# Kernel optimization log

Hardware: AMD Instinct MI355X
Metric: run time of the kernel (lower is better)

Reference implementation:

```python
import jax, jax.numpy as jnp
import numpy as np

N, H, E = 40000, 128, 640000
BN_EPS = 1e-5


def setup_inputs() -> dict:
    key = jax.random.key(0)
    ks = jax.random.split(key, 5)
    x = jax.random.normal(ks[0], (N, H), dtype=jnp.float32)
    edge_index = jax.random.randint(ks[1], (2, E), 0, N, dtype=jnp.int64)
    eps = jnp.zeros((1,), dtype=jnp.float32)
    s = 1.0 / np.sqrt(H)  # torch Linear init scale
    W1 = jax.random.uniform(ks[2], (H, H), jnp.float32, -s, s)
    b1 = jnp.zeros((H,), dtype=jnp.float32)
    W2 = jax.random.uniform(ks[3], (H, H), jnp.float32, -s, s)
    b2 = jnp.zeros((H,), dtype=jnp.float32)
    gamma = jnp.ones((H,), dtype=jnp.float32)
    beta = jnp.zeros((H,), dtype=jnp.float32)
    return {"x": x, "edge_index": edge_index, "eps": eps,
            "W1": W1, "b1": b1, "W2": W2, "b2": b2,
            "gamma": gamma, "beta": beta}


def reference(x, edge_index, eps, W1, b1, W2, b2, gamma, beta):
    src = edge_index[0]
    tgt = edge_index[1]
    # gather source features, scatter-add into target rows: [N, H]
    agg = jax.ops.segment_sum(x[src], tgt, num_segments=x.shape[0])
    out = agg + (1.0 + eps) * x
    # MLP: Linear -> ReLU -> Linear -> BatchNorm1d (train mode) -> ReLU
    h = jax.nn.relu(out @ W1.T + b1)
    h = h @ W2.T + b2
    mean = jnp.mean(h, axis=0)
    var = jnp.mean((h - mean) ** 2, axis=0)  # biased var, as BN uses
    h = (h - mean) * jax.lax.rsqrt(var + BN_EPS) * gamma + beta
    return jax.nn.relu(h)
```

## Files before the change

kernel.cpp:

```cpp
#include <hip/hip_runtime.h>

#define HDIM 128
#define BN_EPS 1e-5f
#define SCAN_BINS 1024
#define NPART 8
#define LSTR 136

typedef short short8 __attribute__((ext_vector_type(8)));
typedef float floatx4 __attribute__((ext_vector_type(4)));

__device__ __forceinline__ unsigned short f2b(float f) {
    union { float f; unsigned u; } v; v.f = f;
    unsigned r = v.u + 0x7FFFu + ((v.u >> 16) & 1u);
    return (unsigned short)(r >> 16);
}

__device__ __forceinline__ float b2f(unsigned short b) {
    union { unsigned u; float f; } v; v.u = (unsigned)b << 16;
    return v.f;
}

__global__ __launch_bounds__(256) void prep_kernel(
    const float* __restrict__ x, unsigned short* __restrict__ xB, long n4,
    const float* __restrict__ W1, const float* __restrict__ W2,
    unsigned short* __restrict__ W1B, unsigned short* __restrict__ W2B,
    const int* __restrict__ eidx, int* __restrict__ hist,
    int* __restrict__ rank, int E)
{
    int tid = blockIdx.x * 256 + threadIdx.x;
    int stride = gridDim.x * 256;
    for (long i = tid; i < n4; i += stride) {
        float4 v = ((const float4*)x)[i];
        ushort4 o;
        o.x = f2b(v.x); o.y = f2b(v.y); o.z = f2b(v.z); o.w = f2b(v.w);
        ((ushort4*)xB)[i] = o;
    }
    for (int i = tid; i < HDIM * HDIM; i += stride) {
        W1B[i] = f2b(W1[i]);
        W2B[i] = f2b(W2[i]);
    }
    for (int e = tid; e < E; e += stride) {
        rank[e] = atomicAdd(&hist[eidx[E + e]], 1);
    }
}

__global__ __launch_bounds__(256) void block_scan_kernel(
    const int* __restrict__ hist, int* __restrict__ offsets,
    int* __restrict__ blockSums, float* __restrict__ statSum, int N)
{
    __shared__ int ts[256];
    int b = blockIdx.x, t = threadIdx.x;
    if (b == 0 && t < 2 * HDIM) statSum[t] = 0.f;
    int base = b * SCAN_BINS + t * 4;
    int4 h = make_int4(0, 0, 0, 0);
    if (base + 3 < N) {
        h = *(const int4*)(hist + base);
    } else {
        if (base + 0 < N) h.x = hist[base + 0];
        if (base + 1 < N) h.y = hist[base + 1];
        if (base + 2 < N) h.z = hist[base + 2];
    }
    int s = h.x + h.y + h.z + h.w;
    ts[t] = s;
    __syncthreads();
    for (int off = 1; off < 256; off <<= 1) {
        int v = ts[t];
        int add = (t >= off) ? ts[t - off] : 0;
        __syncthreads();
        ts[t] = v + add;
        __syncthreads();
    }
    int excl = ts[t] - s;
    int4 o;
    o.x = excl;
    o.y = o.x + h.x;
    o.z = o.y + h.y;
    o.w = o.z + h.z;
    if (base + 3 < N) {
        *(int4*)(offsets + base) = o;
    } else {
        if (base + 0 < N) offsets[base + 0] = o.x;
        if (base + 1 < N) offsets[base + 1] = o.y;
        if (base + 2 < N) offsets[base + 2] = o.z;
    }
    if (t == 255) blockSums[b] = ts[255];
}

__global__ __launch_bounds__(256) void scan_finalize_kernel(
    const int* __restrict__ blockSums, int* __restrict__ offsets, int N, int NB)
{
    __shared__ int ts[256];
    int b = blockIdx.x, t = threadIdx.x;
    ts[t] = (t < NB) ? blockSums[t] : 0;
    __syncthreads();
    for (int off = 1; off < 256; off <<= 1) {
        int v = ts[t];
        int add = (t >= off) ? ts[t - off] : 0;
        __syncthreads();
        ts[t] = v + add;
        __syncthreads();
    }
    int prefix = (b == 0) ? 0 : ts[b - 1];
    if (b == 0 && t == 0) offsets[N] = ts[NB - 1];
    int base = b * SCAN_BINS + t * 4;
    if (base + 3 < N) {
        int4 o = *(int4*)(offsets + base);
        o.x += prefix; o.y += prefix; o.z += prefix; o.w += prefix;
        *(int4*)(offsets + base) = o;
    } else {
        for (int j = 0; j < 4; j++) {
            int i = base + j;
            if (i < N) offsets[i] += prefix;
        }
    }
}

__global__ __launch_bounds__(256) void reorder_kernel(
    const int* __restrict__ eidx, const int* __restrict__ offsets,
    const int* __restrict__ rank, int* __restrict__ srcSorted,
    int E, int partSize)
{
    int part = blockIdx.x & (NPART - 1);
    int bi = blockIdx.x >> 3;
    int nb = gridDim.x >> 3;
    int lo = part * partSize;
    int hi = lo + partSize;
    int stride = nb * 256;
    for (int e = bi * 256 + threadIdx.x; e < E; e += stride) {
        int t = eidx[E + e];
        if (t >= lo && t < hi) {
            srcSorted[offsets[t] + rank[e]] = eidx[e];
        }
    }
}

__global__ __launch_bounds__(256, 4) void mega_kernel(
    const float* __restrict__ x, const unsigned short* __restrict__ xB,
    const int* __restrict__ offsets, const int* __restrict__ srcSorted,
    const float* __restrict__ eps,
    const unsigned short* __restrict__ W1B, const float* __restrict__ b1,
    const unsigned short* __restrict__ W2B, const float* __restrict__ b2,
    float* __restrict__ out, float* __restrict__ statSum,
    float* __restrict__ statSqs, int N)
{
    __shared__ unsigned short sT[64 * LSTR];
    __shared__ float sSum[HDIM];
    __shared__ float sSqs[HDIM];

    int tid = threadIdx.x;
    int rb = blockIdx.x * 64;
    if (tid < HDIM) { sSum[tid] = 0.f; sSqs[tid] = 0.f; }

    float coef = 1.0f + eps[0];
    int tx = tid & 15, ty = tid >> 4;
    int col = tx * 8;
    for (int g = 0; g < 4; g++) {
        int r = g * 16 + ty;
        int row = rb + r;
        float acc[8] = {0.f, 0.f, 0.f, 0.f, 0.f, 0.f, 0.f, 0.f};
        if (row < N) {
            float4 xv0 = *(const float4*)(x + (size_t)row * HDIM + col);
            float4 xv1 = *(const float4*)(x + (size_t)row * HDIM + col + 4);
            acc[0] = coef * xv0.x; acc[1] = coef * xv0.y;
            acc[2] = coef * xv0.z; acc[3] = coef * xv0.w;
            acc[4] = coef * xv1.x; acc[5] = coef * xv1.y;
            acc[6] = coef * xv1.z; acc[7] = coef * xv1.w;
            int beg = offsets[row], end = offsets[row + 1];
            int e = beg;
            for (; e + 7 < end; e += 8) {
                short8 u[8];
                #pragma unroll
                for (int q = 0; q < 8; q++) {
                    int s = srcSorted[e + q];
                    u[q] = *(const short8*)(xB + (size_t)s * HDIM + col);
                }
                #pragma unroll
                for (int q = 0; q < 8; q++)
                    #pragma unroll
                    for (int j = 0; j < 8; j++)
                        acc[j] += b2f((unsigned short)u[q][j]);
            }
            for (; e < end; e++) {
                int s = srcSorted[e];
                short8 u = *(const short8*)(xB + (size_t)s * HDIM + col);
                #pragma unroll
                for (int j = 0; j < 8; j++)
                    acc[j] += b2f((unsigned short)u[j]);
            }
        }
        short8 o;
        #pragma unroll
        for (int j = 0; j < 8; j++) o[j] = (short)f2b(acc[j]);
        *(short8*)(sT + r * LSTR + col) = o;
    }
    __syncthreads();

    int w = tid >> 6;
    int l = tid & 63;
    int m = l & 15, quad = l >> 4;
    unsigned short* myT = sT + w * 16 * LSTR;

    floatx4 acc1[8];
    #pragma unroll
    for (int t = 0; t < 8; t++) acc1[t] = (floatx4){0.f, 0.f, 0.f, 0.f};
    #pragma unroll
    for (int kk = 0; kk < 4; kk++) {
        int k0 = kk * 32 + quad * 8;
        short8 a = *(const short8*)(myT + m * LSTR + k0);
        #pragma unroll
        for (int t = 0; t < 8; t++) {
            short8 bfr = *(const short8*)(W1B + (size_t)(t * 16 + m) * HDIM + k0);
            acc1[t] = __builtin_amdgcn_mfma_f32_16x16x32_bf16(a, bfr, acc1[t], 0, 0, 0);
        }
    }
    #pragma unroll
    for (int t = 0; t < 8; t++) {
        int colc = t * 16 + m;
        float bs = b1[colc];
        #pragma unroll
        for (int r = 0; r < 4; r++) {
            float v = fmaxf(acc1[t][r] + bs, 0.f);
            myT[(quad * 4 + r) * LSTR + colc] = f2b(v);
        }
    }

    floatx4 acc2[8];
    #pragma unroll
    for (int t = 0; t < 8; t++) acc2[t] = (floatx4){0.f, 0.f, 0.f, 0.f};
    #pragma unroll
    for (int kk = 0; kk < 4; kk++) {
        int k0 = kk * 32 + quad * 8;
        short8 a = *(const short8*)(myT + m * LSTR + k0);
        #pragma unroll
        for (int t = 0; t < 8; t++) {
            short8 bfr = *(const short8*)(W2B + (size_t)(t * 16 + m) * HDIM + k0);
            acc2[t] = __builtin_amdgcn_mfma_f32_16x16x32_bf16(a, bfr, acc2[t], 0, 0, 0);
        }
    }
    int row0 = rb + w * 16 + quad * 4;
    #pragma unroll
    for (int t = 0; t < 8; t++) {
        int colc = t * 16 + m;
        float bs = b2[colc];
        float cs = 0.f, cq = 0.f;
        #pragma unroll
        for (int r = 0; r < 4; r++) {
            int row = row0 + r;
            if (row < N) {
                float v = acc2[t][r] + bs;
                out[(size_t)row * HDIM + colc] = v;
                cs += v; cq += v * v;
            }
        }
        cs += __shfl_xor(cs, 16, 64);
        cs += __shfl_xor(cs, 32, 64);
        cq += __shfl_xor(cq, 16, 64);
        cq += __shfl_xor(cq, 32, 64);
        if (quad == 0) {
            atomicAdd(&sSum[colc], cs);
            atomicAdd(&sSqs[colc], cq);
        }
    }
    __syncthreads();
    if (tid < HDIM) {
        atomicAdd(&statSum[tid], sSum[tid]);
        atomicAdd(&statSqs[tid], sSqs[tid]);
    }
}

__global__ __launch_bounds__(256) void bn_apply_kernel(
    float* __restrict__ out, const float* __restrict__ statSum,
    const float* __restrict__ statSqs, const float* __restrict__ gamma,
    const float* __restrict__ beta, int N, long n4)
{
    __shared__ float sSc[HDIM];
    __shared__ float sSh[HDIM];
    int t = threadIdx.x;
    if (t < HDIM) {
        float invN = 1.0f / (float)N;
        float mean = statSum[t] * invN;
        float var = statSqs[t] * invN - mean * mean;
        float sc = gamma[t] * rsqrtf(var + BN_EPS);
        sSc[t] = sc;
        sSh[t] = beta[t] - mean * sc;
    }
    __syncthreads();
    long stride = (long)gridDim.x * 256;
    for (long i = (long)blockIdx.x * 256 + t; i < n4; i += stride) {
        int cg = (int)(i & 31) * 4;
        float4 v = ((float4*)out)[i];
        v.x = fmaxf(v.x * sSc[cg + 0] + sSh[cg + 0], 0.f);
        v.y = fmaxf(v.y * sSc[cg + 1] + sSh[cg + 1], 0.f);
        v.z = fmaxf(v.z * sSc[cg + 2] + sSh[cg + 2], 0.f);
        v.w = fmaxf(v.w * sSc[cg + 3] + sSh[cg + 3], 0.f);
        ((float4*)out)[i] = v;
    }
}

extern "C" void kernel_launch(void* const* d_in, const int* in_sizes, int n_in,
                              void* d_out, int out_size, void* d_ws, size_t ws_size,
                              hipStream_t stream) {
    const float* x     = (const float*)d_in[0];
    const int*   eidx  = (const int*)d_in[1];
    const float* eps   = (const float*)d_in[2];
    const float* W1    = (const float*)d_in[3];
    const float* b1    = (const float*)d_in[4];
    const float* W2    = (const float*)d_in[5];
    const float* b2    = (const float*)d_in[6];
    const float* gamma = (const float*)d_in[7];
    const float* beta  = (const float*)d_in[8];
    float* out = (float*)d_out;

    int N = in_sizes[0] / HDIM;
    int E = in_sizes[1] / 2;
    size_t NH = (size_t)N * HDIM;
    int NB = (N + SCAN_BINS - 1) / SCAN_BINS;
    int NpadOff = (N + 1 + 3) & ~3;
    int partSize = (N + NPART - 1) / NPART;
    long n4 = (long)NH / 4;

    unsigned short* xB   = (unsigned short*)d_ws;
    unsigned short* W1B  = xB + NH;
    unsigned short* W2B  = W1B + HDIM * HDIM;
    float* statSum = (float*)(W2B + HDIM * HDIM);
    float* statSqs = statSum + HDIM;
    int*   hist    = (int*)(statSqs + HDIM);
    int*   offsets = hist + N;
    int*   rank    = offsets + NpadOff;
    int*   srcSorted = rank + E;
    int*   blockSums = srcSorted + E;

    hipMemsetAsync(hist, 0, (size_t)N * sizeof(int), stream);
    prep_kernel<<<1280, 256, 0, stream>>>(x, xB, n4, W1, W2, W1B, W2B, eidx, hist, rank, E);
    block_scan_kernel<<<NB, 256, 0, stream>>>(hist, offsets, blockSums, statSum, N);
    scan_finalize_kernel<<<NB, 256, 0, stream>>>(blockSums, offsets, N, NB);
    reorder_kernel<<<2048, 256, 0, stream>>>(eidx, offsets, rank, srcSorted, E, partSize);
    int gblocks = (N + 63) / 64;
    mega_kernel<<<gblocks, 256, 0, stream>>>(
        x, xB, offsets, srcSorted, eps, W1B, b1, W2B, b2,
        out, statSum, statSqs, N);
    bn_apply_kernel<<<2048, 256, 0, stream>>>(
        out, statSum, statSqs, gamma, beta, N, n4);
}
```

Baseline: 201.4 us.

## Slab-partition bf16 features for gather locality and merge scan kernels

Stores the bf16 copy of x as four 32-column slabs ([slab][node][32]). The aggregation kernel now gives each row to 4 lanes that walk all edges once per slab, so each slab pass touches a smaller working set that can stay in cache. The self term now reads the bf16 slab instead of fp32 x, which adds rounding on that term. The two-pass scan becomes a single kernel where each block recomputes its prefix by summing the earlier histogram entries, dropping a launch at the cost of redundant reads.

```diff
diff --git a/kernel.cpp b/kernel.cpp
--- a/kernel.cpp
+++ b/kernel.cpp
@@ -4,6 +4,7 @@
 #define BN_EPS 1e-5f
 #define SCAN_BINS 1024
 #define NPART 8
+#define NSLAB 4
 #define LSTR 136
 
 typedef short short8 __attribute__((ext_vector_type(8)));
@@ -21,7 +22,7 @@
 }
 
 __global__ __launch_bounds__(256) void prep_kernel(
-    const float* __restrict__ x, unsigned short* __restrict__ xB, long n4,
+    const float* __restrict__ x, unsigned short* __restrict__ xS, int N,
     const float* __restrict__ W1, const float* __restrict__ W2,
     unsigned short* __restrict__ W1B, unsigned short* __restrict__ W2B,
     const int* __restrict__ eidx, int* __restrict__ hist,
@@ -29,11 +30,22 @@
 {
     int tid = blockIdx.x * 256 + threadIdx.x;
     int stride = gridDim.x * 256;
-    for (long i = tid; i < n4; i += stride) {
-        float4 v = ((const float4*)x)[i];
-        ushort4 o;
-        o.x = f2b(v.x); o.y = f2b(v.y); o.z = f2b(v.z); o.w = f2b(v.w);
-        ((ushort4*)xB)[i] = o;
+    long n8 = (long)N * (HDIM / 8);
+    for (long i = tid; i < n8; i += stride) {
+        int n = (int)(i >> 4);
+        int u = (int)(i & 15);
+        int c = u * 8;
+        int s = c >> 5;
+        int off = c & 31;
+        const float* src = x + (size_t)n * HDIM + c;
+        float4 v0 = *(const float4*)(src);
+        float4 v1 = *(const float4*)(src + 4);
+        short8 o;
+        o[0] = (short)f2b(v0.x); o[1] = (short)f2b(v0.y);
+        o[2] = (short)f2b(v0.z); o[3] = (short)f2b(v0.w);
+        o[4] = (short)f2b(v1.x); o[5] = (short)f2b(v1.y);
+        o[6] = (short)f2b(v1.z); o[7] = (short)f2b(v1.w);
+        *(short8*)(xS + ((size_t)s * N + n) * 32 + off) = o;
     }
     for (int i = tid; i < HDIM * HDIM; i += stride) {
         W1B[i] = f2b(W1[i]);
@@ -44,13 +56,26 @@
     }
 }
 
-__global__ __launch_bounds__(256) void block_scan_kernel(
+__global__ __launch_bounds__(256) void scan_kernel(
     const int* __restrict__ hist, int* __restrict__ offsets,
-    int* __restrict__ blockSums, float* __restrict__ statSum, int N)
+    float* __restrict__ statSum, int N, int NB)
 {
     __shared__ int ts[256];
     int b = blockIdx.x, t = threadIdx.x;
     if (b == 0 && t < 2 * HDIM) statSum[t] = 0.f;
+
+    int lim = b * SCAN_BINS;
+    int pre = 0;
+    for (int i = t; i < lim; i += 256) pre += hist[i];
+    ts[t] = pre;
+    __syncthreads();
+    for (int off = 128; off > 0; off >>= 1) {
+        if (t < off) ts[t] += ts[t + off];
+        __syncthreads();
+    }
+    int blockPrefix = ts[0];
+    __syncthreads();
+
     int base = b * SCAN_BINS + t * 4;
     int4 h = make_int4(0, 0, 0, 0);
     if (base + 3 < N) {
@@ -70,7 +95,7 @@
         ts[t] = v + add;
         __syncthreads();
     }
-    int excl = ts[t] - s;
+    int excl = blockPrefix + ts[t] - s;
     int4 o;
     o.x = excl;
     o.y = o.x + h.x;
@@ -83,36 +108,7 @@
         if (base + 1 < N) offsets[base + 1] = o.y;
         if (base + 2 < N) offsets[base + 2] = o.z;
     }
-    if (t == 255) blockSums[b] = ts[255];
-}
-
-__global__ __launch_bounds__(256) void scan_finalize_kernel(
-    const int* __restrict__ blockSums, int* __restrict__ offsets, int N, int NB)
-{
-    __shared__ int ts[256];
-    int b = blockIdx.x, t = threadIdx.x;
-    ts[t] = (t < NB) ? blockSums[t] : 0;
-    __syncthreads();
-    for (int off = 1; off < 256; off <<= 1) {
-        int v = ts[t];
-        int add = (t >= off) ? ts[t - off] : 0;
-        __syncthreads();
-        ts[t] = v + add;
-        __syncthreads();
-    }
-    int prefix = (b == 0) ? 0 : ts[b - 1];
-    if (b == 0 && t == 0) offsets[N] = ts[NB - 1];
-    int base = b * SCAN_BINS + t * 4;
-    if (base + 3 < N) {
-        int4 o = *(int4*)(offsets + base);
-        o.x += prefix; o.y += prefix; o.z += prefix; o.w += prefix;
-        *(int4*)(offsets + base) = o;
-    } else {
-        for (int j = 0; j < 4; j++) {
-            int i = base + j;
-            if (i < N) offsets[i] += prefix;
-        }
-    }
+    if (b == NB - 1 && t == 255) offsets[N] = blockPrefix + ts[255];
 }
 
 __global__ __launch_bounds__(256) void reorder_kernel(
@@ -135,7 +131,7 @@
 }
 
 __global__ __launch_bounds__(256, 4) void mega_kernel(
-    const float* __restrict__ x, const unsigned short* __restrict__ xB,
+    const unsigned short* __restrict__ xS,
     const int* __restrict__ offsets, const int* __restrict__ srcSorted,
     const float* __restrict__ eps,
     const unsigned short* __restrict__ W1B, const float* __restrict__ b1,
@@ -152,46 +148,49 @@
     if (tid < HDIM) { sSum[tid] = 0.f; sSqs[tid] = 0.f; }
 
     float coef = 1.0f + eps[0];
-    int tx = tid & 15, ty = tid >> 4;
-    int col = tx * 8;
-    for (int g = 0; g < 4; g++) {
-        int r = g * 16 + ty;
-        int row = rb + r;
+    int rloc = tid >> 2;
+    int lane4 = tid & 3;
+    int cis = lane4 * 8;
+    int row = rb + rloc;
+    int beg = 0, end = 0;
+    if (row < N) { beg = offsets[row]; end = offsets[row + 1]; }
+
+    #pragma unroll
+    for (int s = 0; s < NSLAB; s++) {
+        const unsigned short* slab = xS + (size_t)s * N * 32;
         float acc[8] = {0.f, 0.f, 0.f, 0.f, 0.f, 0.f, 0.f, 0.f};
+        int e = beg;
+        for (; e + 3 < end; e += 4) {
+            int i0 = srcSorted[e];
+            int i1 = srcSorted[e + 1];
+            int i2 = srcSorted[e + 2];
+            int i3 = srcSorted[e + 3];
+            short8 u0 = *(const short8*)(slab + (size_t)i0 * 32 + cis);
+            short8 u1 = *(const short8*)(slab + (size_t)i1 * 32 + cis);
+            short8 u2 = *(const short8*)(slab + (size_t)i2 * 32 + cis);
+            short8 u3 = *(const short8*)(slab + (size_t)i3 * 32 + cis);
+            #pragma unroll
+            for (int j = 0; j < 8; j++)
+                acc[j] += (b2f((unsigned short)u0[j]) + b2f((unsigned short)u1[j]))
+                        + (b2f((unsigned short)u2[j]) + b2f((unsigned short)u3[j]));
+        }
+        for (; e < end; e++) {
+            int si = srcSorted[e];
+            short8 u = *(const short8*)(slab + (size_t)si * 32 + cis);
+            #pragma unroll
+            for (int j = 0; j < 8; j++)
+                acc[j] += b2f((unsigned short)u[j]);
+        }
         if (row < N) {
-            float4 xv0 = *(const float4*)(x + (size_t)row * HDIM + col);
-            float4 xv1 = *(const float4*)(x + (size_t)row * HDIM + col + 4);
-            acc[0] = coef * xv0.x; acc[1] = coef * xv0.y;
-            acc[2] = coef * xv0.z; acc[3] = coef * xv0.w;
-            acc[4] = coef * xv1.x; acc[5] = coef * xv1.y;
-            acc[6] = coef * xv1.z; acc[7] = coef * xv1.w;
-            int beg = offsets[row], end = offsets[row + 1];
-            int e = beg;
-            for (; e + 7 < end; e += 8) {
-                short8 u[8];
-                #pragma unroll
-                for (int q = 0; q < 8; q++) {
-                    int s = srcSorted[e + q];
-                    u[q] = *(const short8*)(xB + (size_t)s * HDIM + col);
-                }
-                #pragma unroll
-                for (int q = 0; q < 8; q++)
-                    #pragma unroll
-                    for (int j = 0; j < 8; j++)
-                        acc[j] += b2f((unsigned short)u[q][j]);
-            }
-            for (; e < end; e++) {
-                int s = srcSorted[e];
-                short8 u = *(const short8*)(xB + (size_t)s * HDIM + col);
-                #pragma unroll
-                for (int j = 0; j < 8; j++)
-                    acc[j] += b2f((unsigned short)u[j]);
-            }
+            short8 us = *(const short8*)(slab + (size_t)row * 32 + cis);
+            #pragma unroll
+            for (int j = 0; j < 8; j++)
+                acc[j] += coef * b2f((unsigned short)us[j]);
         }
         short8 o;
         #pragma unroll
         for (int j = 0; j < 8; j++) o[j] = (short)f2b(acc[j]);
-        *(short8*)(sT + r * LSTR + col) = o;
+        *(short8*)(sT + rloc * LSTR + s * 32 + cis) = o;
     }
     __syncthreads();
 
@@ -245,10 +244,10 @@
         float cs = 0.f, cq = 0.f;
         #pragma unroll
         for (int r = 0; r < 4; r++) {
-            int row = row0 + r;
-            if (row < N) {
+            int rw = row0 + r;
+            if (rw < N) {
                 float v = acc2[t][r] + bs;
-                out[(size_t)row * HDIM + colc] = v;
+                out[(size_t)rw * HDIM + colc] = v;
                 cs += v; cq += v * v;
             }
         }
@@ -319,8 +318,8 @@
     int partSize = (N + NPART - 1) / NPART;
     long n4 = (long)NH / 4;
 
-    unsigned short* xB   = (unsigned short*)d_ws;
-    unsigned short* W1B  = xB + NH;
+    unsigned short* xS   = (unsigned short*)d_ws;
+    unsigned short* W1B  = xS + NH;
     unsigned short* W2B  = W1B + HDIM * HDIM;
     float* statSum = (float*)(W2B + HDIM * HDIM);
     float* statSqs = statSum + HDIM;
@@ -328,16 +327,14 @@
     int*   offsets = hist + N;
     int*   rank    = offsets + NpadOff;
     int*   srcSorted = rank + E;
-    int*   blockSums = srcSorted + E;
 
     hipMemsetAsync(hist, 0, (size_t)N * sizeof(int), stream);
-    prep_kernel<<<1280, 256, 0, stream>>>(x, xB, n4, W1, W2, W1B, W2B, eidx, hist, rank, E);
-    block_scan_kernel<<<NB, 256, 0, stream>>>(hist, offsets, blockSums, statSum, N);
-    scan_finalize_kernel<<<NB, 256, 0, stream>>>(blockSums, offsets, N, NB);
+    prep_kernel<<<1280, 256, 0, stream>>>(x, xS, N, W1, W2, W1B, W2B, eidx, hist, rank, E);
+    scan_kernel<<<NB, 256, 0, stream>>>(hist, offsets, statSum, N, NB);
     reorder_kernel<<<2048, 256, 0, stream>>>(eidx, offsets, rank, srcSorted, E, partSize);
     int gblocks = (N + 63) / 64;
     mega_kernel<<<gblocks, 256, 0, stream>>>(
-        x, xB, offsets, srcSorted, eps, W1B, b1, W2B, b2,
+        xS, offsets, srcSorted, eps, W1B, b1, W2B, b2,
         out, statSum, statSqs, N);
     bn_apply_kernel<<<2048, 256, 0, stream>>>(
         out, statSum, statSqs, gamma, beta, N, n4);
```

Result: slower. 219.3 us (+8.9%).

## Fuse CSR prefix scan into reorder kernel and read bf16 self features

Applied to the files above, without the earlier changes.

The two-pass block scan and finalize kernels plus the separate reorder kernel are replaced, when a partition fits in shared memory, by one kernel in which each block recomputes its partition's prefix and offsets in LDS and then scatters source indices using those LDS offsets. This removes two launches and the global offsets round trip during reorder, at the cost of redundant histogram reads across blocks. The mega kernel now takes the self term from the bf16 copy of x instead of fp32 x, which halves that read but reduces precision of the (1+eps)*x term. Zeroing of the BN stats moves into prep_kernel.

```diff
diff --git a/kernel.cpp b/kernel.cpp
--- a/kernel.cpp
+++ b/kernel.cpp
@@ -4,6 +4,7 @@
 #define BN_EPS 1e-5f
 #define SCAN_BINS 1024
 #define NPART 8
+#define MAXPART 5120
 #define LSTR 136
 
 typedef short short8 __attribute__((ext_vector_type(8)));
@@ -25,10 +26,11 @@
     const float* __restrict__ W1, const float* __restrict__ W2,
     unsigned short* __restrict__ W1B, unsigned short* __restrict__ W2B,
     const int* __restrict__ eidx, int* __restrict__ hist,
-    int* __restrict__ rank, int E)
+    int* __restrict__ rank, float* __restrict__ statSum, int E)
 {
     int tid = blockIdx.x * 256 + threadIdx.x;
     int stride = gridDim.x * 256;
+    if (tid < 2 * HDIM) statSum[tid] = 0.f;
     for (long i = tid; i < n4; i += stride) {
         float4 v = ((const float4*)x)[i];
         ushort4 o;
@@ -44,13 +46,85 @@
     }
 }
 
-__global__ __launch_bounds__(256) void block_scan_kernel(
-    const int* __restrict__ hist, int* __restrict__ offsets,
-    int* __restrict__ blockSums, float* __restrict__ statSum, int N)
-{
+__global__ __launch_bounds__(256) void scan_reorder_kernel(
+    const int* __restrict__ hist, const int* __restrict__ eidx,
+    const int* __restrict__ rank, int* __restrict__ offsets,
+    int* __restrict__ srcSorted, int N, int E, int partSize)
+{
+    __shared__ int sOff[MAXPART];
     __shared__ int ts[256];
     int b = blockIdx.x, t = threadIdx.x;
-    if (b == 0 && t < 2 * HDIM) statSum[t] = 0.f;
+    int part = b & (NPART - 1);
+    int bi = b >> 3;
+    int nb = gridDim.x >> 3;
+    int lo = part * partSize;
+    int hi = lo + partSize; if (hi > N) hi = N;
+    int len = hi - lo;
+
+    int pre = 0;
+    for (int i = t; i < lo; i += 256) pre += hist[i];
+    ts[t] = pre;
+    __syncthreads();
+    for (int off = 128; off > 0; off >>= 1) {
+        if (t < off) ts[t] += ts[t + off];
+        __syncthreads();
+    }
+    int prefix = ts[0];
+    __syncthreads();
+
+    for (int i = t; i < len; i += 256) sOff[i] = hist[lo + i];
+    __syncthreads();
+
+    int chunk = (len + 255) / 256;
+    int clo = t * chunk;
+    int chi = clo + chunk; if (chi > len) chi = len;
+    int s = 0;
+    for (int i = clo; i < chi; i++) s += sOff[i];
+    ts[t] = s;
+    __syncthreads();
+    for (int off = 1; off < 256; off <<= 1) {
+        int v = ts[t];
+        int add = (t >= off) ? ts[t - off] : 0;
+        __syncthreads();
+        ts[t] = v + add;
+        __syncthreads();
+    }
+    int excl = prefix + ts[t] - s;
+    for (int i = clo; i < chi; i++) {
+        int v = sOff[i];
+        sOff[i] = excl;
+        if (bi == 0) offsets[lo + i] = excl;
+        excl += v;
+    }
+    if (bi == 0 && part == NPART - 1 && t == 0) offsets[N] = E;
+    __syncthreads();
+
+    int stride = nb * 256;
+    for (int e = bi * 256 + t; e < E; e += stride) {
+        int tg = eidx[E + e];
+        if (tg >= lo && tg < hi) {
+            srcSorted[sOff[tg - lo] + rank[e]] = eidx[e];
+        }
+    }
+}
+
+__global__ __launch_bounds__(256) void scan_kernel(
+    const int* __restrict__ hist, int* __restrict__ offsets,
+    int N, int NB)
+{
+    __shared__ int ts[256];
+    int b = blockIdx.x, t = threadIdx.x;
+    int lim = b * SCAN_BINS;
+    int pre = 0;
+    for (int i = t; i < lim; i += 256) pre += hist[i];
+    ts[t] = pre;
+    __syncthreads();
+    for (int off = 128; off > 0; off >>= 1) {
+        if (t < off) ts[t] += ts[t + off];
+        __syncthreads();
+    }
+    int blockPrefix = ts[0];
+    __syncthreads();
     int base = b * SCAN_BINS + t * 4;
     int4 h = make_int4(0, 0, 0, 0);
     if (base + 3 < N) {
@@ -70,7 +144,7 @@
         ts[t] = v + add;
         __syncthreads();
     }
-    int excl = ts[t] - s;
+    int excl = blockPrefix + ts[t] - s;
     int4 o;
     o.x = excl;
     o.y = o.x + h.x;
@@ -83,36 +157,7 @@
         if (base + 1 < N) offsets[base + 1] = o.y;
         if (base + 2 < N) offsets[base + 2] = o.z;
     }
-    if (t == 255) blockSums[b] = ts[255];
-}
-
-__global__ __launch_bounds__(256) void scan_finalize_kernel(
-    const int* __restrict__ blockSums, int* __restrict__ offsets, int N, int NB)
-{
-    __shared__ int ts[256];
-    int b = blockIdx.x, t = threadIdx.x;
-    ts[t] = (t < NB) ? blockSums[t] : 0;
-    __syncthreads();
-    for (int off = 1; off < 256; off <<= 1) {
-        int v = ts[t];
-        int add = (t >= off) ? ts[t - off] : 0;
-        __syncthreads();
-        ts[t] = v + add;
-        __syncthreads();
-    }
-    int prefix = (b == 0) ? 0 : ts[b - 1];
-    if (b == 0 && t == 0) offsets[N] = ts[NB - 1];
-    int base = b * SCAN_BINS + t * 4;
-    if (base + 3 < N) {
-        int4 o = *(int4*)(offsets + base);
-        o.x += prefix; o.y += prefix; o.z += prefix; o.w += prefix;
-        *(int4*)(offsets + base) = o;
-    } else {
-        for (int j = 0; j < 4; j++) {
-            int i = base + j;
-            if (i < N) offsets[i] += prefix;
-        }
-    }
+    if (b == NB - 1 && t == 255) offsets[N] = blockPrefix + ts[255];
 }
 
 __global__ __launch_bounds__(256) void reorder_kernel(
@@ -135,7 +180,7 @@
 }
 
 __global__ __launch_bounds__(256, 4) void mega_kernel(
-    const float* __restrict__ x, const unsigned short* __restrict__ xB,
+    const unsigned short* __restrict__ xB,
     const int* __restrict__ offsets, const int* __restrict__ srcSorted,
     const float* __restrict__ eps,
     const unsigned short* __restrict__ W1B, const float* __restrict__ b1,
@@ -159,12 +204,9 @@
         int row = rb + r;
         float acc[8] = {0.f, 0.f, 0.f, 0.f, 0.f, 0.f, 0.f, 0.f};
         if (row < N) {
-            float4 xv0 = *(const float4*)(x + (size_t)row * HDIM + col);
-            float4 xv1 = *(const float4*)(x + (size_t)row * HDIM + col + 4);
-            acc[0] = coef * xv0.x; acc[1] = coef * xv0.y;
-            acc[2] = coef * xv0.z; acc[3] = coef * xv0.w;
-            acc[4] = coef * xv1.x; acc[5] = coef * xv1.y;
-            acc[6] = coef * xv1.z; acc[7] = coef * xv1.w;
+            short8 us = *(const short8*)(xB + (size_t)row * HDIM + col);
+            #pragma unroll
+            for (int j = 0; j < 8; j++) acc[j] = coef * b2f((unsigned short)us[j]);
             int beg = offsets[row], end = offsets[row + 1];
             int e = beg;
             for (; e + 7 < end; e += 8) {
@@ -245,10 +287,10 @@
         float cs = 0.f, cq = 0.f;
         #pragma unroll
         for (int r = 0; r < 4; r++) {
-            int row = row0 + r;
-            if (row < N) {
+            int rw = row0 + r;
+            if (rw < N) {
                 float v = acc2[t][r] + bs;
-                out[(size_t)row * HDIM + colc] = v;
+                out[(size_t)rw * HDIM + colc] = v;
                 cs += v; cq += v * v;
             }
         }
@@ -328,16 +370,19 @@
     int*   offsets = hist + N;
     int*   rank    = offsets + NpadOff;
     int*   srcSorted = rank + E;
-    int*   blockSums = srcSorted + E;
 
     hipMemsetAsync(hist, 0, (size_t)N * sizeof(int), stream);
-    prep_kernel<<<1280, 256, 0, stream>>>(x, xB, n4, W1, W2, W1B, W2B, eidx, hist, rank, E);
-    block_scan_kernel<<<NB, 256, 0, stream>>>(hist, offsets, blockSums, statSum, N);
-    scan_finalize_kernel<<<NB, 256, 0, stream>>>(blockSums, offsets, N, NB);
-    reorder_kernel<<<2048, 256, 0, stream>>>(eidx, offsets, rank, srcSorted, E, partSize);
+    prep_kernel<<<1280, 256, 0, stream>>>(x, xB, n4, W1, W2, W1B, W2B, eidx, hist, rank, statSum, E);
+    if (partSize <= MAXPART) {
+        scan_reorder_kernel<<<256, 256, 0, stream>>>(
+            hist, eidx, rank, offsets, srcSorted, N, E, partSize);
+    } else {
+        scan_kernel<<<NB, 256, 0, stream>>>(hist, offsets, N, NB);
+        reorder_kernel<<<2048, 256, 0, stream>>>(eidx, offsets, rank, srcSorted, E, partSize);
+    }
     int gblocks = (N + 63) / 64;
     mega_kernel<<<gblocks, 256, 0, stream>>>(
-        x, xB, offsets, srcSorted, eps, W1B, b1, W2B, b2,
+        xB, offsets, srcSorted, eps, W1B, b1, W2B, b2,
         out, statSum, statSqs, N);
     bn_apply_kernel<<<2048, 256, 0, stream>>>(
         out, statSum, statSqs, gamma, beta, N, n4);
```

Result: slower. 253.9 us (+26.1%).
